# Performance work log

Hardware: AMD Instinct MI355X
Metric: run time of the kernel (lower is better)

## Reference

```python
import jax, jax.numpy as jnp
import numpy as np

EPS = 1e-6
SINKHORN_ITERS = 8
TEMPERATURE = 1.0
B, N, D = 4, 8192, 512
E, OUT = 8, 512
H = 1


def setup_inputs() -> dict:
    key = jax.random.key(0)
    k1, k2, k3 = jax.random.split(key, 3)
    x = jax.random.normal(k1, (B, N, D), dtype=jnp.float32)
    gate_weight = jax.random.normal(k2, (H, D, E), dtype=jnp.float32)
    experts = jax.random.normal(k3, (E, D, OUT), dtype=jnp.float32) * 0.02
    return {"x": x, "gate_weight": gate_weight, "experts": experts}


def _sinkhorn(logits):
    # logits: (b, h, n, e). log(clamp(.,eps)) then alternating row/col log-normalization.
    t = jnp.log(jnp.clip(logits, EPS)) / TEMPERATURE
    for _ in range(SINKHORN_ITERS):
        t = t - jax.nn.logsumexp(t, axis=-2, keepdims=True)  # normalize over tokens n
        t = t - jax.nn.logsumexp(t, axis=-1, keepdims=True)  # normalize over experts e
    return jnp.exp(t)


def reference(x, gate_weight, experts):
    b, n, d = x.shape
    e = experts.shape[0]
    m = n // e  # tokens per expert
    xh = x[:, None, :, :]  # b 1 n d  (single-headed -> h=1)
    gate_logits = jnp.einsum('bhnd,hde->bhne', xh, gate_weight)
    gates = _sinkhorn(gate_logits)  # b h n e
    # topk over token dim n, per expert: move n to last axis for lax.top_k
    g_t = jnp.swapaxes(gates, -1, -2)  # b h e n
    vals, idx = jax.lax.top_k(g_t, m)  # (b h e m), (b h e m)
    gate_values = jnp.transpose(vals, (2, 0, 1, 3))[..., None]  # e b h m 1
    # gather routed tokens: routed[e,b,h,m,d] = x[b,h,idx[b,h,e,m],d]
    routed = jnp.take_along_axis(xh[:, :, None, :, :], idx[..., None], axis=3)  # b h e m d
    routed = jnp.transpose(routed, (2, 0, 1, 3, 4))  # e b h m d
    expert_w = experts[:, None, :, :]  # e h i o with h=1 (rearrange 'e i o -> e 1 i o')
    outputs = jnp.einsum('ebhmi,ehio->ebhmo', routed, expert_w)  # e b h m o
    outputs = outputs * gate_values
    # scatter back (set semantics, matching einx set_at)
    bh_idx = idx.reshape(b, 1, e * m)  # b h (e m)
    bh_vals = jnp.transpose(outputs, (1, 2, 0, 3, 4)).reshape(b, 1, e * m, outputs.shape[-1])
    def scat(i1, v1):
        return jnp.zeros((n, v1.shape[-1]), dtype=v1.dtype).at[i1].set(v1)
    routed_back = jax.vmap(jax.vmap(scat))(bh_idx, bh_vals)  # b h n o
    return routed_back[:, 0]  # b n o
```

## Files before the change

kernel.cpp:

```cpp
#include <hip/hip_runtime.h>
#include <hip/hip_bf16.h>

#define BB 4
#define NN 8192
#define DD 512
#define EE 8
#define OUTD 512
#define TOPM 1024
#define EPSV 1e-6f
#define ITERS 8

using s16x8 = __attribute__((ext_vector_type(8))) short;
using f32x4 = __attribute__((ext_vector_type(4))) float;
typedef unsigned long long u64;

__device__ __forceinline__ unsigned short f2bf(float f) {
  unsigned u = __float_as_uint(f);
  return (unsigned short)((u + 0x7FFFu + ((u >> 16) & 1u)) >> 16);
}

__device__ __forceinline__ void gll16(const void* g, void* l) {
  __builtin_amdgcn_global_load_lds((const __attribute__((address_space(1))) void*)g,
                                   (__attribute__((address_space(3))) void*)l, 16, 0, 0);
}

__global__ __launch_bounds__(256) void k_gate(const float* __restrict__ x,
                                              const float* __restrict__ gw,
                                              float* __restrict__ t0,
                                              unsigned short* __restrict__ xbf,
                                              int* __restrict__ eo,
                                              int* __restrict__ counts,
                                              const float* __restrict__ W,
                                              unsigned short* __restrict__ WT) {
  const int tid = threadIdx.x;
  if (blockIdx.x >= 1024) {
    __shared__ float tl[32][33];
    const int widx = blockIdx.x - 1024;
    const int e = widx >> 8, rem = widx & 255;
    const int k0 = (rem >> 4) * 32, n0 = (rem & 15) * 32;
    const int ty = tid >> 5, tx = tid & 31;
    const float* src = W + ((long)e * DD + k0) * OUTD + n0;
#pragma unroll
    for (int j = 0; j < 4; ++j)
      tl[ty + j * 8][tx] = src[(long)(ty + j * 8) * OUTD + tx];
    __syncthreads();
    unsigned short* dst = WT + ((long)e * OUTD + n0) * DD + k0;
#pragma unroll
    for (int j = 0; j < 4; ++j)
      dst[(long)(ty + j * 8) * DD + tx] = f2bf(tl[tx][ty + j * 8]);
    return;
  }
  if (tid < 32) eo[blockIdx.x * 32 + tid] = -1;
  if (blockIdx.x == 0 && tid >= 64 && tid < 64 + BB * EE) counts[tid - 64] = 0;
  const int lane = tid & 63;
  const int w    = tid >> 6;
  float4 g0[8], g1[8];
  const float* gb = gw + (lane * 8) * EE;
#pragma unroll
  for (int q = 0; q < 8; ++q) {
    g0[q] = *(const float4*)(gb + q * EE);
    g1[q] = *(const float4*)(gb + q * EE + 4);
  }
  const long row0 = (long)blockIdx.x * 32 + w * 8;
  for (int i = 0; i < 8; ++i) {
    const long row = row0 + i;
    const float* xr = x + row * DD + lane * 8;
    float4 xa = *(const float4*)(xr);
    float4 xb = *(const float4*)(xr + 4);
    float xv[8] = {xa.x, xa.y, xa.z, xa.w, xb.x, xb.y, xb.z, xb.w};
    s16x8 xo;
#pragma unroll
    for (int j = 0; j < 8; ++j) xo[j] = (short)f2bf(xv[j]);
    *(s16x8*)(xbf + row * DD + lane * 8) = xo;

    float acc[8] = {0.f,0.f,0.f,0.f,0.f,0.f,0.f,0.f};
#pragma unroll
    for (int q = 0; q < 8; ++q) {
      acc[0] += xv[q] * g0[q].x; acc[1] += xv[q] * g0[q].y;
      acc[2] += xv[q] * g0[q].z; acc[3] += xv[q] * g0[q].w;
      acc[4] += xv[q] * g1[q].x; acc[5] += xv[q] * g1[q].y;
      acc[6] += xv[q] * g1[q].z; acc[7] += xv[q] * g1[q].w;
    }
#pragma unroll
    for (int d = 1; d <= 4; d <<= 1) {
#pragma unroll
      for (int e = 0; e < 8; ++e) {
        float tmp = __shfl_xor(acc[e], d);
        acc[e] += ((lane & d) == (e & d)) ? tmp : 0.f;
      }
    }
    float v = acc[0];
#pragma unroll
    for (int e = 1; e < 8; ++e) v = ((lane & 7) == e) ? acc[e] : v;
#pragma unroll
    for (int d = 8; d < 64; d <<= 1) v += __shfl_xor(v, d);
    if (lane < 8) t0[row * EE + lane] = logf(fmaxf(v, EPSV));
  }
}

__global__ __launch_bounds__(1024) void k_sink5(const float* __restrict__ t0,
                                                float* __restrict__ R,
                                                float* __restrict__ C) {
  const int b = blockIdx.x;
  const int tid = threadIdx.x;
  const int wv = tid >> 6, ln = tid & 63;
  const float* tb = t0 + (long)b * NN * EE;
  float E[8][8], u[8], dl[8];
  __shared__ float ws[16][8];
  __shared__ float Csh[8];
  __shared__ float Ssh[8];
#pragma unroll
  for (int j = 0; j < 8; ++j) {
    const float* p = tb + (long)(j * 1024 + tid) * EE;
    float4 a = *(const float4*)p, b4 = *(const float4*)(p + 4);
    E[j][0] = expf(a.x);  E[j][1] = expf(a.y);
    E[j][2] = expf(a.z);  E[j][3] = expf(a.w);
    E[j][4] = expf(b4.x); E[j][5] = expf(b4.y);
    E[j][6] = expf(b4.z); E[j][7] = expf(b4.w);
    u[j] = 1.f;
  }
  for (int it = 0; it < ITERS; ++it) {
    float P[8] = {0.f,0.f,0.f,0.f,0.f,0.f,0.f,0.f};
#pragma unroll
    for (int j = 0; j < 8; ++j)
#pragma unroll
      for (int e = 0; e < 8; ++e) P[e] += E[j][e] * u[j];
#pragma unroll
    for (int d = 1; d <= 4; d <<= 1) {
#pragma unroll
      for (int e = 0; e < 8; ++e) {
        float tmp = __shfl_xor(P[e], d);
        P[e] += ((ln & d) == (e & d)) ? tmp : 0.f;
      }
    }
    float pv = P[0];
#pragma unroll
    for (int e = 1; e < 8; ++e) pv = ((ln & 7) == e) ? P[e] : pv;
#pragma unroll
    for (int d = 8; d < 64; d <<= 1) pv += __shfl_xor(pv, d);
    if (ln < 8) ws[wv][ln] = pv;
    __syncthreads();
    if (tid < 64) {
      const int q = ln >> 3, e = ln & 7;
      float s = ws[q][e] + ws[q + 8][e];
#pragma unroll
      for (int d = 8; d < 64; d <<= 1) s += __shfl_xor(s, d);
      if (ln < 8) { Csh[ln] = 1.f / s; Ssh[ln] = s; }
    }
    __syncthreads();
    float vv[8];
#pragma unroll
    for (int e = 0; e < 8; ++e) vv[e] = Csh[e];
#pragma unroll
    for (int j = 0; j < 8; ++j) {
      float d0 = E[j][0] * vv[0];
#pragma unroll
      for (int e = 1; e < 8; ++e) d0 += E[j][e] * vv[e];
      dl[j] = d0;
      u[j] = 1.f / d0;
    }
    __syncthreads();
  }
#pragma unroll
  for (int j = 0; j < 8; ++j) R[(long)b * NN + j * 1024 + tid] = logf(dl[j]);
  if (tid < 8) C[b * EE + tid] = logf(Ssh[tid]);
}

__global__ __launch_bounds__(1024) void k_topk(const float* __restrict__ t0,
                                               const float* __restrict__ R,
                                               int* __restrict__ expert_of) {
  __shared__ unsigned key[NN];
  __shared__ int hist[256];
  __shared__ int bcast[2];
  __shared__ int wsum[16];
  const int b = blockIdx.x >> 3, e = blockIdx.x & 7;
  const int tid = threadIdx.x;
  const int wv = tid >> 6, ln = tid & 63;
  const float* t = t0 + (long)b * NN * EE + e;
  const float* Rb = R + b * NN;
  for (int n = tid; n < NN; n += 1024) {
    float f = t[n * EE] - Rb[n];
    unsigned u = __float_as_uint(f);
    u = (u & 0x80000000u) ? ~u : (u | 0x80000000u);
    key[n] = u;
  }
  __syncthreads();
  unsigned prefix = 0, mask = 0;
  int k = TOPM;
  for (int shift = 24; shift >= 0; shift -= 8) {
    if (tid < 256) hist[tid] = 0;
    __syncthreads();
    for (int n = tid; n < NN; n += 1024) {
      unsigned u = key[n];
      if ((u & mask) == prefix) atomicAdd(&hist[(u >> shift) & 255], 1);
    }
    __syncthreads();
    for (int d = 1; d < 256; d <<= 1) {
      int add = 0;
      if (tid < 256 - d) add = hist[tid + d];
      __syncthreads();
      if (tid < 256) hist[tid] += add;
      __syncthreads();
    }
    if (tid < 256) {
      int sv = hist[tid];
      int sv1 = (tid < 255) ? hist[tid + 1] : 0;
      if (sv >= k && sv1 < k) { bcast[0] = k - sv1; bcast[1] = tid; }
    }
    __syncthreads();
    k = bcast[0];
    prefix |= ((unsigned)bcast[1]) << shift;
    mask |= (255u << shift);
    __syncthreads();
  }
  const unsigned theta = prefix;
  const int need = k;
  const int base = tid * 8;
  int c = 0;
#pragma unroll
  for (int j = 0; j < 8; ++j) if (key[base + j] == theta) ++c;
  int inc = c;
#pragma unroll
  for (int d = 1; d < 64; d <<= 1) {
    int o = __shfl_up(inc, d);
    if (ln >= d) inc += o;
  }
  if (ln == 63) wsum[wv] = inc;
  __syncthreads();
  if (tid == 0) {
    int runv = 0;
    for (int i = 0; i < 16; ++i) { int t2 = wsum[i]; wsum[i] = runv; runv += t2; }
  }
  __syncthreads();
  int run = wsum[wv] + inc - c;
  int* eo = expert_of + b * NN;
  for (int j = 0; j < 8; ++j) {
    int n = base + j;
    unsigned u = key[n];
    bool sel = false;
    if (u > theta) sel = true;
    else if (u == theta) { if (run < need) sel = true; ++run; }
    if (sel) atomicMax(&eo[n], e);
  }
}

__global__ __launch_bounds__(256) void k_build(const int* __restrict__ expert_of,
                                               const float* __restrict__ t0,
                                               const float* __restrict__ R,
                                               const float* __restrict__ C,
                                               int* __restrict__ counts,
                                               int* __restrict__ lists,
                                               float* __restrict__ gvals) {
  __shared__ int hist8[8], base8[8];
  const int tid = threadIdx.x;
  if (tid < 8) hist8[tid] = 0;
  __syncthreads();
  const long i = (long)blockIdx.x * 256 + tid;
  const int b = (int)(i >> 13);
  const int e = expert_of[i];
  int lpos = -1;
  if (e >= 0) lpos = atomicAdd(&hist8[e], 1);
  __syncthreads();
  if (tid < 8 && hist8[tid] > 0)
    base8[tid] = atomicAdd(&counts[b * EE + tid], hist8[tid]);
  __syncthreads();
  if (e >= 0) {
    const int n = (int)(i & (NN - 1));
    const int be = b * EE + e;
    const int slot = be * TOPM + base8[e] + lpos;
    lists[slot] = n;
    gvals[slot] = expf(t0[i * EE + e] - C[be] - R[i]);
  }
}

__global__ __launch_bounds__(256) void k_zero(const int* __restrict__ eo,
                                              float* __restrict__ out) {
  const int row = blockIdx.x * 4 + (threadIdx.x >> 6);
  if (eo[row] >= 0) return;
  const int ln = threadIdx.x & 63;
  float4 z = make_float4(0.f, 0.f, 0.f, 0.f);
  float4* p = (float4*)(out + (long)row * OUTD) + ln;
  p[0] = z; p[64] = z;
}

__global__ __launch_bounds__(256) void k_gemm(const unsigned short* __restrict__ xbf,
                                              const unsigned short* __restrict__ WT,
                                              const int* __restrict__ counts,
                                              const int* __restrict__ lists,
                                              const float* __restrict__ gvals,
                                              float* __restrict__ out) {
  const int be = blockIdx.z;
  const int b = be >> 3, e = be & 7;
  const int cnt = counts[be];
  const int r0 = blockIdx.y * 128;
  if (r0 >= cnt) return;
  const int c0 = blockIdx.x * 128;

  __shared__ unsigned short As[128 * 32];
  __shared__ unsigned short Bs[128 * 32];
  __shared__ int   rowTok[128];
  __shared__ float rowG[128];

  const int tid = threadIdx.x;
  if (tid < 128) {
    int r = r0 + tid;
    rowTok[tid] = (r < cnt) ? lists[be * TOPM + r] : -1;
    rowG[tid]   = (r < cnt) ? gvals[be * TOPM + r] : 0.f;
  }
  __syncthreads();

  const int w = tid >> 6, l = tid & 63;
  const int c_a = 2 * w, c_b = 2 * w + 1;
  const int rr = l >> 2;
  const int slot = l & 3;
  const int ra0 = c_a * 16 + rr;
  const int ra1 = c_b * 16 + rr;
  const int kg0 = slot ^ ((ra0 >> 1) & 3);
  const int kg1 = slot ^ ((ra1 >> 1) & 3);
  int tA0 = rowTok[ra0]; if (tA0 < 0) tA0 = 0;
  int tA1 = rowTok[ra1]; if (tA1 < 0) tA1 = 0;
  const unsigned short* gA0 = xbf + ((long)b * NN + tA0) * DD + kg0 * 8;
  const unsigned short* gA1 = xbf + ((long)b * NN + tA1) * DD + kg1 * 8;
  const unsigned short* gB0 = WT + ((long)e * OUTD + c0 + ra0) * DD + kg0 * 8;
  const unsigned short* gB1 = WT + ((long)e * OUTD + c0 + ra1) * DD + kg1 * 8;
  unsigned short* lA0 = As + c_a * 512;
  unsigned short* lA1 = As + c_b * 512;
  unsigned short* lB0 = Bs + c_a * 512;
  unsigned short* lB1 = Bs + c_b * 512;

  const int wr = w >> 1, wc = w & 1;
  const int fr = l & 15, fq = l >> 4;
  int aoff[4], boff[4];
#pragma unroll
  for (int m = 0; m < 4; ++m) {
    int row = wr * 64 + m * 16 + fr;
    aoff[m] = row * 32 + (fq ^ ((row >> 1) & 3)) * 8;
    int col = wc * 64 + m * 16 + fr;
    boff[m] = col * 32 + (fq ^ ((col >> 1) & 3)) * 8;
  }

  f32x4 acc[4][4] = {};

  gll16(gA0, lA0); gll16(gA1, lA1);
  gll16(gB0, lB0); gll16(gB1, lB1);

  for (int ks = 0; ks < 16; ++ks) {
    __syncthreads();
    s16x8 af[4], bfr[4];
#pragma unroll
    for (int m = 0; m < 4; ++m) af[m] = *(const s16x8*)(As + aoff[m]);
#pragma unroll
    for (int n = 0; n < 4; ++n) bfr[n] = *(const s16x8*)(Bs + boff[n]);
    __syncthreads();
    if (ks < 15) {
      int off = (ks + 1) * 32;
      gll16(gA0 + off, lA0); gll16(gA1 + off, lA1);
      gll16(gB0 + off, lB0); gll16(gB1 + off, lB1);
    }
#pragma unroll
    for (int m = 0; m < 4; ++m)
#pragma unroll
      for (int n = 0; n < 4; ++n)
        acc[m][n] = __builtin_amdgcn_mfma_f32_16x16x32_bf16(af[m], bfr[n], acc[m][n], 0, 0, 0);
  }

#pragma unroll
  for (int m = 0; m < 4; ++m) {
    int rbase = wr * 64 + m * 16 + fq * 4;
    int tok[4]; float g[4];
#pragma unroll
    for (int j = 0; j < 4; ++j) { tok[j] = rowTok[rbase + j]; g[j] = rowG[rbase + j]; }
#pragma unroll
    for (int n = 0; n < 4; ++n) {
      int col = c0 + wc * 64 + n * 16 + fr;
#pragma unroll
      for (int j = 0; j < 4; ++j) {
        if (tok[j] >= 0)
          out[((long)b * NN + tok[j]) * OUTD + col] = acc[m][n][j] * g[j];
      }
    }
  }
}

extern "C" void kernel_launch(void* const* d_in, const int* in_sizes, int n_in,
                              void* d_out, int out_size, void* d_ws, size_t ws_size,
                              hipStream_t stream) {
  const float* x  = (const float*)d_in[0];
  const float* gw = (const float*)d_in[1];
  const float* ex = (const float*)d_in[2];
  float* out = (float*)d_out;

  char* wsb = (char*)d_ws;
  float*          t0     = (float*)(wsb);
  unsigned short* xbf    = (unsigned short*)(wsb + (1l << 20));
  unsigned short* WT     = (unsigned short*)(wsb + (33l << 20));
  const long base = 37l << 20;
  float*          R      = (float*)(wsb + base);
  int*            eo     = (int*)  (wsb + base + (128l << 10));
  int*            lists  = (int*)  (wsb + base + (256l << 10));
  float*          gvals  = (float*)(wsb + base + (384l << 10));
  float*          C      = (float*)(wsb + base + (512l << 10));
  int*            counts = (int*)  (wsb + base + (512l << 10) + 1024);

  k_gate<<<1024 + 2048, 256, 0, stream>>>(x, gw, t0, xbf, eo, counts, ex, WT);
  k_sink5<<<BB, 1024, 0, stream>>>(t0, R, C);
  k_topk<<<BB * EE, 1024, 0, stream>>>(t0, R, eo);
  k_build<<<(BB * NN) / 256, 256, 0, stream>>>(eo, t0, R, C, counts, lists, gvals);
  k_zero<<<(BB * NN) / 4, 256, 0, stream>>>(eo, out);
  k_gemm<<<dim3(OUTD / 128, TOPM / 128, BB * EE), 256, 0, stream>>>(xbf, WT, counts, lists, gvals, out);
}
```

Baseline: 123.5 us.

## Double the GEMM K-tile to 64 and remap blocks to a flat grid

The expert GEMM now stages 64-wide K slices (8 iterations instead of 16), with a new 8-way XOR swizzle and load mapping. This halves the number of barrier pairs and LDS refill rounds per tile. The 3D grid becomes a 1D grid with row-tile index fastest, so blocks sharing the same weight columns run close together. LDS use per block doubles, which may reduce occupancy.

```diff
diff --git a/kernel.cpp b/kernel.cpp
--- a/kernel.cpp
+++ b/kernel.cpp
@@ -289,15 +289,18 @@
                                               const int* __restrict__ lists,
                                               const float* __restrict__ gvals,
                                               float* __restrict__ out) {
-  const int be = blockIdx.z;
+  const int id = blockIdx.x;
+  const int xq = id >> 8;
+  const int be = (id >> 3) & 31;
+  const int yq = id & 7;
   const int b = be >> 3, e = be & 7;
   const int cnt = counts[be];
-  const int r0 = blockIdx.y * 128;
+  const int r0 = yq * 128;
   if (r0 >= cnt) return;
-  const int c0 = blockIdx.x * 128;
-
-  __shared__ unsigned short As[128 * 32];
-  __shared__ unsigned short Bs[128 * 32];
+  const int c0 = xq * 128;
+
+  __shared__ unsigned short As[128 * 64];
+  __shared__ unsigned short Bs[128 * 64];
   __shared__ int   rowTok[128];
   __shared__ float rowG[128];
 
@@ -310,66 +313,77 @@
   __syncthreads();
 
   const int w = tid >> 6, l = tid & 63;
-  const int c_a = 2 * w, c_b = 2 * w + 1;
-  const int rr = l >> 2;
-  const int slot = l & 3;
-  const int ra0 = c_a * 16 + rr;
-  const int ra1 = c_b * 16 + rr;
-  const int kg0 = slot ^ ((ra0 >> 1) & 3);
-  const int kg1 = slot ^ ((ra1 >> 1) & 3);
-  int tA0 = rowTok[ra0]; if (tA0 < 0) tA0 = 0;
-  int tA1 = rowTok[ra1]; if (tA1 < 0) tA1 = 0;
-  const unsigned short* gA0 = xbf + ((long)b * NN + tA0) * DD + kg0 * 8;
-  const unsigned short* gA1 = xbf + ((long)b * NN + tA1) * DD + kg1 * 8;
-  const unsigned short* gB0 = WT + ((long)e * OUTD + c0 + ra0) * DD + kg0 * 8;
-  const unsigned short* gB1 = WT + ((long)e * OUTD + c0 + ra1) * DD + kg1 * 8;
-  unsigned short* lA0 = As + c_a * 512;
-  unsigned short* lA1 = As + c_b * 512;
-  unsigned short* lB0 = Bs + c_a * 512;
-  unsigned short* lB1 = Bs + c_b * 512;
+  const int rbase = w * 32 + (l >> 3);
+  const int sL = l & 7;
+  const unsigned short* xb_b = xbf + (long)b * NN * DD;
+  const unsigned short* wt_e = WT + (long)e * OUTD * DD;
+  int tokc[4]; int sGa[4], sGb[4];
+#pragma unroll
+  for (int c = 0; c < 4; ++c) {
+    int r = rbase + c * 8;
+    int tk = rowTok[r]; if (tk < 0) tk = 0;
+    tokc[c] = tk;
+    sGa[c] = (sL ^ (r & 7)) * 8;
+    sGb[c] = sGa[c];
+  }
 
   const int wr = w >> 1, wc = w & 1;
   const int fr = l & 15, fq = l >> 4;
-  int aoff[4], boff[4];
+  int aoff[4][2], boff[4][2];
 #pragma unroll
   for (int m = 0; m < 4; ++m) {
-    int row = wr * 64 + m * 16 + fr;
-    aoff[m] = row * 32 + (fq ^ ((row >> 1) & 3)) * 8;
-    int col = wc * 64 + m * 16 + fr;
-    boff[m] = col * 32 + (fq ^ ((col >> 1) & 3)) * 8;
+#pragma unroll
+    for (int kk = 0; kk < 2; ++kk) {
+      int row = wr * 64 + m * 16 + fr;
+      aoff[m][kk] = row * 64 + (((fq + 4 * kk) ^ (row & 7)) * 8);
+      int col = wc * 64 + m * 16 + fr;
+      boff[m][kk] = col * 64 + (((fq + 4 * kk) ^ (col & 7)) * 8);
+    }
   }
 
   f32x4 acc[4][4] = {};
 
-  gll16(gA0, lA0); gll16(gA1, lA1);
-  gll16(gB0, lB0); gll16(gB1, lB1);
-
-  for (int ks = 0; ks < 16; ++ks) {
-    __syncthreads();
-    s16x8 af[4], bfr[4];
-#pragma unroll
-    for (int m = 0; m < 4; ++m) af[m] = *(const s16x8*)(As + aoff[m]);
-#pragma unroll
-    for (int n = 0; n < 4; ++n) bfr[n] = *(const s16x8*)(Bs + boff[n]);
-    __syncthreads();
-    if (ks < 15) {
-      int off = (ks + 1) * 32;
-      gll16(gA0 + off, lA0); gll16(gA1 + off, lA1);
-      gll16(gB0 + off, lB0); gll16(gB1 + off, lB1);
-    }
-#pragma unroll
-    for (int m = 0; m < 4; ++m)
-#pragma unroll
-      for (int n = 0; n < 4; ++n)
-        acc[m][n] = __builtin_amdgcn_mfma_f32_16x16x32_bf16(af[m], bfr[n], acc[m][n], 0, 0, 0);
-  }
+#define STAGE(kb) {                                                          \
+    int ko = (kb) * 64;                                                      \
+    _Pragma("unroll")                                                        \
+    for (int c = 0; c < 4; ++c) {                                            \
+      int r = rbase + c * 8;                                                 \
+      gll16(xb_b + (long)tokc[c] * DD + ko + sGa[c],                         \
+            As + (w * 32 + c * 8) * 64);                                     \
+      gll16(wt_e + (long)(c0 + r) * DD + ko + sGb[c],                        \
+            Bs + (w * 32 + c * 8) * 64);                                     \
+    }                                                                        \
+  }
+
+  STAGE(0);
+  for (int kb = 0; kb < 8; ++kb) {
+    __syncthreads();
+    s16x8 af[4][2], bf_[4][2];
+#pragma unroll
+    for (int m = 0; m < 4; ++m) {
+      af[m][0] = *(const s16x8*)(As + aoff[m][0]);
+      af[m][1] = *(const s16x8*)(As + aoff[m][1]);
+      bf_[m][0] = *(const s16x8*)(Bs + boff[m][0]);
+      bf_[m][1] = *(const s16x8*)(Bs + boff[m][1]);
+    }
+    __syncthreads();
+    if (kb < 7) STAGE(kb + 1);
+#pragma unroll
+    for (int kk = 0; kk < 2; ++kk)
+#pragma unroll
+      for (int m = 0; m < 4; ++m)
+#pragma unroll
+        for (int n = 0; n < 4; ++n)
+          acc[m][n] = __builtin_amdgcn_mfma_f32_16x16x32_bf16(af[m][kk], bf_[n][kk], acc[m][n], 0, 0, 0);
+  }
+#undef STAGE
 
 #pragma unroll
   for (int m = 0; m < 4; ++m) {
-    int rbase = wr * 64 + m * 16 + fq * 4;
+    int rbase2 = wr * 64 + m * 16 + fq * 4;
     int tok[4]; float g[4];
 #pragma unroll
-    for (int j = 0; j < 4; ++j) { tok[j] = rowTok[rbase + j]; g[j] = rowG[rbase + j]; }
+    for (int j = 0; j < 4; ++j) { tok[j] = rowTok[rbase2 + j]; g[j] = rowG[rbase2 + j]; }
 #pragma unroll
     for (int n = 0; n < 4; ++n) {
       int col = c0 + wc * 64 + n * 16 + fr;
@@ -407,5 +421,5 @@
   k_topk<<<BB * EE, 1024, 0, stream>>>(t0, R, eo);
   k_build<<<(BB * NN) / 256, 256, 0, stream>>>(eo, t0, R, C, counts, lists, gvals);
   k_zero<<<(BB * NN) / 4, 256, 0, stream>>>(eo, out);
-  k_gemm<<<dim3(OUTD / 128, TOPM / 128, BB * EE), 256, 0, stream>>>(xbf, WT, counts, lists, gvals, out);
-}
+  k_gemm<<<1024, 256, 0, stream>>>(xbf, WT, counts, lists, gvals, out);
+}
```

Result: faster. 118.9 us (-3.7%).
